# Optimization experiments

Hardware: AMD Instinct MI355X
Metric: run time of the kernel (lower is better)

## Reference

```python
import jax, jax.numpy as jnp
import numpy as np

B, D, S, SEQ_MAX = 8, 256, 1024, 1028  # seq_max = 4*seq_len+4 with seq_len=256
EPS = 1e-5


def setup_inputs() -> dict:
    key = jax.random.key(0)
    k1, k2 = jax.random.split(key, 2)
    x = jax.random.normal(k1, (B, D, S), dtype=jnp.float32)
    weight = jax.random.normal(k2, (D, SEQ_MAX, SEQ_MAX), dtype=jnp.float32)
    gamma = jnp.ones((D,), dtype=jnp.float32)   # LayerNorm weight
    beta = jnp.zeros((D,), dtype=jnp.float32)   # LayerNorm bias
    return {"x": x, "weight": weight, "gamma": gamma, "beta": beta}


def reference(x, weight, gamma, beta):
    s = x.shape[2]
    # strictly-causal per-channel mixing matrix (tril, diagonal=-1)
    w = jnp.tril(weight[:, :s, :s], k=-1)            # [d, s, s]
    # c[b,d,i] = sum_w x[b,d,w] * w[d,i,w]
    c = jax.nn.relu(jnp.einsum('bdw,diw->bdi', x, w))  # [b, d, s]
    # bracket(c, x, 0): elementwise multiplicative gating
    y = x + c * x
    # LayerNorm over the channel (d_model) axis, as in permute->LN->permute
    mu = jnp.mean(y, axis=1, keepdims=True)
    var = jnp.mean((y - mu) ** 2, axis=1, keepdims=True)
    yhat = (y - mu) * jax.lax.rsqrt(var + EPS)
    return yhat * gamma[None, :, None] + beta[None, :, None]
```

## Files before the change

kernel.cpp:

```cpp
#include <hip/hip_runtime.h>

#define SM 1028
#define D_ 256
#define S_ 1024
#define B_ 8

__global__ __launch_bounds__(256, 4)
void lie_mix_kernel(const float* __restrict__ x, const float* __restrict__ weight,
                    float* __restrict__ y) {
  int bid = blockIdx.x;
  int d = bid & 255;
  int bi = 15 - (bid >> 8);
  int i0 = bi << 6;

  __shared__ float xs[B_][S_];

  int t = threadIdx.x;
  int wlim4 = (i0 + 64) >> 2;
  for (int bb = 0; bb < B_; ++bb) {
    const float4* src = (const float4*)(x + ((size_t)bb * D_ + d) * S_);
    float4* dst = (float4*)(&xs[bb][0]);
    for (int idx = t; idx < wlim4; idx += 256) dst[idx] = src[idx];
  }
  __syncthreads();

  int lane = t & 63;
  int wid = t >> 6;
  int g = lane >> 4;
  int jj = lane & 15;
  int rbase = i0 + wid * 16 + g * 4;

  const float* wbase = weight + ((size_t)d * SM + rbase) * SM + 4 * jj;

  float acc[4][8];
#pragma unroll
  for (int k = 0; k < 4; ++k)
#pragma unroll
    for (int b = 0; b < 8; ++b) acc[k][b] = 0.f;

  int F = i0 >> 6;

  float4 wc[4];
#pragma unroll
  for (int k = 0; k < 4; ++k) wc[k] = *(const float4*)(wbase + (size_t)k * SM);

  for (int c = 0; c < F; ++c) {
    float4 wn[4];
    const float* p = wbase + (c + 1) * 64;
#pragma unroll
    for (int k = 0; k < 4; ++k) wn[k] = *(const float4*)(p + (size_t)k * SM);
    int w0 = c * 64;
#pragma unroll
    for (int b = 0; b < 8; ++b) {
      float4 xb = *(const float4*)&xs[b][w0 + 4 * jj];
#pragma unroll
      for (int k = 0; k < 4; ++k) {
        acc[k][b] += xb.x * wc[k].x;
        acc[k][b] += xb.y * wc[k].y;
        acc[k][b] += xb.z * wc[k].z;
        acc[k][b] += xb.w * wc[k].w;
      }
    }
#pragma unroll
    for (int k = 0; k < 4; ++k) wc[k] = wn[k];
  }

  {
    int lim_base = wid * 16 + g * 4;
    float4 wm[4];
#pragma unroll
    for (int k = 0; k < 4; ++k) {
      int lim = lim_base + k;
      wm[k].x = (4 * jj + 0 < lim) ? wc[k].x : 0.f;
      wm[k].y = (4 * jj + 1 < lim) ? wc[k].y : 0.f;
      wm[k].z = (4 * jj + 2 < lim) ? wc[k].z : 0.f;
      wm[k].w = (4 * jj + 3 < lim) ? wc[k].w : 0.f;
    }
#pragma unroll
    for (int b = 0; b < 8; ++b) {
      float4 xb = *(const float4*)&xs[b][i0 + 4 * jj];
#pragma unroll
      for (int k = 0; k < 4; ++k) {
        acc[k][b] += xb.x * wm[k].x;
        acc[k][b] += xb.y * wm[k].y;
        acc[k][b] += xb.z * wm[k].z;
        acc[k][b] += xb.w * wm[k].w;
      }
    }
  }

#pragma unroll
  for (int s = 1; s < 16; s <<= 1) {
#pragma unroll
    for (int k = 0; k < 4; ++k)
#pragma unroll
      for (int b = 0; b < 8; ++b)
        acc[k][b] += __shfl_xor(acc[k][b], s, 64);
  }

  if (jj < 8) {
#pragma unroll
    for (int k = 0; k < 4; ++k) {
      float v = acc[k][0];
#pragma unroll
      for (int b = 1; b < 8; ++b) v = (jj == b) ? acc[k][b] : v;
      float r = fmaxf(v, 0.f);
      float xv = xs[jj][rbase + k];
      y[((size_t)jj * D_ + d) * S_ + rbase + k] = xv * (1.f + r);
    }
  }
}

__global__ __launch_bounds__(256)
void ln_kernel(const float* __restrict__ y, const float* __restrict__ gamma,
               const float* __restrict__ beta, float* __restrict__ out) {
  __shared__ float tile[D_][33];
  __shared__ float ps[8][32];
  __shared__ float pq[8][32];
  __shared__ float mu[32];
  __shared__ float rs[32];
  int b = blockIdx.x >> 5;
  int s0 = (blockIdx.x & 31) << 5;
  int t = threadIdx.x;
  int sj = t & 31, dq = t >> 5;
  for (int dd = dq; dd < D_; dd += 8)
    tile[dd][sj] = y[((size_t)b * D_ + dd) * S_ + s0 + sj];
  __syncthreads();
  float sm = 0.f, sq = 0.f;
#pragma unroll 8
  for (int r = 0; r < 32; ++r) {
    float v = tile[dq * 32 + r][sj];
    sm += v;
    sq += v * v;
  }
  ps[dq][sj] = sm;
  pq[dq][sj] = sq;
  __syncthreads();
  if (t < 32) {
    float S = 0.f, Q = 0.f;
#pragma unroll
    for (int q = 0; q < 8; ++q) { S += ps[q][t]; Q += pq[q][t]; }
    float m = S * (1.f / 256.f);
    float var = Q * (1.f / 256.f) - m * m;
    mu[t] = m;
    rs[t] = rsqrtf(var + 1e-5f);
  }
  __syncthreads();
  for (int dd = dq; dd < D_; dd += 8) {
    float v = tile[dd][sj];
    out[((size_t)b * D_ + dd) * S_ + s0 + sj] =
        (v - mu[sj]) * rs[sj] * gamma[dd] + beta[dd];
  }
}

extern "C" void kernel_launch(void* const* d_in, const int* in_sizes, int n_in,
                              void* d_out, int out_size, void* d_ws, size_t ws_size,
                              hipStream_t stream) {
  const float* x = (const float*)d_in[0];
  const float* weight = (const float*)d_in[1];
  const float* gamma = (const float*)d_in[2];
  const float* beta = (const float*)d_in[3];
  float* out = (float*)d_out;
  float* y = (float*)d_ws;

  lie_mix_kernel<<<4096, 256, 0, stream>>>(x, weight, y);
  ln_kernel<<<256, 256, 0, stream>>>(y, gamma, beta, out);
}
```

Before: 129.1 us.

## Remap mix kernel so each wavefront reads full 1KB weight row segments

Changes the thread mapping of the causal mixing kernel so that all 64 lanes of a wavefront cover 256 contiguous weight columns of one row group, instead of 16 lanes covering 64 columns for four row groups. Each wave now loops over four row quads sequentially and reduces over the full wavefront with six shuffle stages. The x tile load is rounded up to a 256 multiple to match. The aim is wider, more coalesced weight reads. The cost is more shuffle reductions per output, extra lanes doing masked work in the diagonal block, and less parallel independent rows per wave.

Measured after the change: 216.7 us. 1.68x slower.

```diff
diff --git a/kernel.cpp b/kernel.cpp
--- a/kernel.cpp
+++ b/kernel.cpp
@@ -16,7 +16,7 @@
   __shared__ float xs[B_][S_];
 
   int t = threadIdx.x;
-  int wlim4 = (i0 + 64) >> 2;
+  int wlim4 = ((i0 + 64 + 255) & ~255) >> 2;
   for (int bb = 0; bb < B_; ++bb) {
     const float4* src = (const float4*)(x + ((size_t)bb * D_ + d) * S_);
     float4* dst = (float4*)(&xs[bb][0]);
@@ -26,87 +26,98 @@
 
   int lane = t & 63;
   int wid = t >> 6;
-  int g = lane >> 4;
-  int jj = lane & 15;
-  int rbase = i0 + wid * 16 + g * 4;
+  int e0 = lane << 2;
+  const size_t drow = (size_t)d * SM;
 
-  const float* wbase = weight + ((size_t)d * SM + rbase) * SM + 4 * jj;
+  for (int q = 0; q < 4; ++q) {
+    int rq = i0 + ((q << 2) + wid) << 2;
+    rq = i0 + (((q << 2) + wid) << 2);
+    const float* base = weight + (drow + rq) * (size_t)SM;
 
-  float acc[4][8];
+    float acc[4][8];
 #pragma unroll
-  for (int k = 0; k < 4; ++k)
+    for (int k = 0; k < 4; ++k)
 #pragma unroll
-    for (int b = 0; b < 8; ++b) acc[k][b] = 0.f;
+      for (int b = 0; b < 8; ++b) acc[k][b] = 0.f;
 
-  int F = i0 >> 6;
+    int cq = rq >> 8;
 
-  float4 wc[4];
+    float4 wc[4];
+    if (cq > 0) {
 #pragma unroll
-  for (int k = 0; k < 4; ++k) wc[k] = *(const float4*)(wbase + (size_t)k * SM);
+      for (int k = 0; k < 4; ++k)
+        wc[k] = *(const float4*)(base + (size_t)k * SM + e0);
+    }
+    for (int c = 0; c < cq; ++c) {
+      float4 wn[4];
+      if (c + 1 < cq) {
+        const float* p = base + ((c + 1) << 8) + e0;
+#pragma unroll
+        for (int k = 0; k < 4; ++k) wn[k] = *(const float4*)(p + (size_t)k * SM);
+      }
+      int w0 = c << 8;
+#pragma unroll
+      for (int b = 0; b < 8; ++b) {
+        float4 xb = *(const float4*)&xs[b][w0 + e0];
+#pragma unroll
+        for (int k = 0; k < 4; ++k) {
+          acc[k][b] += xb.x * wc[k].x;
+          acc[k][b] += xb.y * wc[k].y;
+          acc[k][b] += xb.z * wc[k].z;
+          acc[k][b] += xb.w * wc[k].w;
+        }
+      }
+      if (c + 1 < cq) {
+#pragma unroll
+        for (int k = 0; k < 4; ++k) wc[k] = wn[k];
+      }
+    }
 
-  for (int c = 0; c < F; ++c) {
-    float4 wn[4];
-    const float* p = wbase + (c + 1) * 64;
-#pragma unroll
-    for (int k = 0; k < 4; ++k) wn[k] = *(const float4*)(p + (size_t)k * SM);
-    int w0 = c * 64;
-#pragma unroll
-    for (int b = 0; b < 8; ++b) {
-      float4 xb = *(const float4*)&xs[b][w0 + 4 * jj];
+    {
+      int w0 = cq << 8;
+      float4 wm[4];
 #pragma unroll
       for (int k = 0; k < 4; ++k) {
-        acc[k][b] += xb.x * wc[k].x;
-        acc[k][b] += xb.y * wc[k].y;
-        acc[k][b] += xb.z * wc[k].z;
-        acc[k][b] += xb.w * wc[k].w;
+        int limit = rq + k - w0;
+        float4 v = make_float4(0.f, 0.f, 0.f, 0.f);
+        if (e0 < limit) v = *(const float4*)(base + (size_t)k * SM + w0 + e0);
+        if (e0 + 1 >= limit) v.y = 0.f;
+        if (e0 + 2 >= limit) v.z = 0.f;
+        if (e0 + 3 >= limit) v.w = 0.f;
+        wm[k] = v;
+      }
+#pragma unroll
+      for (int b = 0; b < 8; ++b) {
+        float4 xb = *(const float4*)&xs[b][w0 + e0];
+#pragma unroll
+        for (int k = 0; k < 4; ++k) {
+          acc[k][b] += xb.x * wm[k].x;
+          acc[k][b] += xb.y * wm[k].y;
+          acc[k][b] += xb.z * wm[k].z;
+          acc[k][b] += xb.w * wm[k].w;
+        }
       }
     }
-#pragma unroll
-    for (int k = 0; k < 4; ++k) wc[k] = wn[k];
-  }
-
-  {
-    int lim_base = wid * 16 + g * 4;
-    float4 wm[4];
-#pragma unroll
-    for (int k = 0; k < 4; ++k) {
-      int lim = lim_base + k;
-      wm[k].x = (4 * jj + 0 < lim) ? wc[k].x : 0.f;
-      wm[k].y = (4 * jj + 1 < lim) ? wc[k].y : 0.f;
-      wm[k].z = (4 * jj + 2 < lim) ? wc[k].z : 0.f;
-      wm[k].w = (4 * jj + 3 < lim) ? wc[k].w : 0.f;
-    }
-#pragma unroll
-    for (int b = 0; b < 8; ++b) {
-      float4 xb = *(const float4*)&xs[b][i0 + 4 * jj];
-#pragma unroll
-      for (int k = 0; k < 4; ++k) {
-        acc[k][b] += xb.x * wm[k].x;
-        acc[k][b] += xb.y * wm[k].y;
-        acc[k][b] += xb.z * wm[k].z;
-        acc[k][b] += xb.w * wm[k].w;
-      }
-    }
-  }
 
 #pragma unroll
-  for (int s = 1; s < 16; s <<= 1) {
+    for (int s = 1; s < 64; s <<= 1) {
+#pragma unroll
+      for (int k = 0; k < 4; ++k)
+#pragma unroll
+        for (int b = 0; b < 8; ++b)
+          acc[k][b] += __shfl_xor(acc[k][b], s, 64);
+    }
+
+    float v = 0.f;
 #pragma unroll
     for (int k = 0; k < 4; ++k)
 #pragma unroll
       for (int b = 0; b < 8; ++b)
-        acc[k][b] += __shfl_xor(acc[k][b], s, 64);
-  }
-
-  if (jj < 8) {
-#pragma unroll
-    for (int k = 0; k < 4; ++k) {
-      float v = acc[k][0];
-#pragma unroll
-      for (int b = 1; b < 8; ++b) v = (jj == b) ? acc[k][b] : v;
-      float r = fmaxf(v, 0.f);
-      float xv = xs[jj][rbase + k];
-      y[((size_t)jj * D_ + d) * S_ + rbase + k] = xv * (1.f + r);
+        v = (lane == (k << 3) + b) ? acc[k][b] : v;
+    if (lane < 32) {
+      int k = lane >> 3, b = lane & 7;
+      float xv = xs[b][rq + k];
+      y[((size_t)b * D_ + d) * S_ + rq + k] = xv * (1.f + fmaxf(v, 0.f));
     }
   }
 }
```

## Drop LDS staging of x, read x directly from global and vectorize output store

Applied to the files above, without the earlier changes.

Removes the 32KB shared-memory tile of x and its barrier, so each thread loads x float4s straight from global/L2 inside the loop. The explicit software prefetch of the next weight chunk is also removed, occupancy hint raised to 5 blocks, the diagonal weight load is masked, and the final output becomes a single float4 store. This aims to cut LDS use and raise occupancy, at the cost of redundant global reads of x across waves and losing the weight double-buffering.

Result: slower. 135.6 us (+5.0%).

```diff
diff --git a/kernel.cpp b/kernel.cpp
--- a/kernel.cpp
+++ b/kernel.cpp
@@ -5,7 +5,7 @@
 #define S_ 1024
 #define B_ 8
 
-__global__ __launch_bounds__(256, 4)
+__global__ __launch_bounds__(256, 5)
 void lie_mix_kernel(const float* __restrict__ x, const float* __restrict__ weight,
                     float* __restrict__ y) {
   int bid = blockIdx.x;
@@ -13,24 +13,16 @@
   int bi = 15 - (bid >> 8);
   int i0 = bi << 6;
 
-  __shared__ float xs[B_][S_];
-
   int t = threadIdx.x;
-  int wlim4 = (i0 + 64) >> 2;
-  for (int bb = 0; bb < B_; ++bb) {
-    const float4* src = (const float4*)(x + ((size_t)bb * D_ + d) * S_);
-    float4* dst = (float4*)(&xs[bb][0]);
-    for (int idx = t; idx < wlim4; idx += 256) dst[idx] = src[idx];
-  }
-  __syncthreads();
-
   int lane = t & 63;
   int wid = t >> 6;
   int g = lane >> 4;
   int jj = lane & 15;
-  int rbase = i0 + wid * 16 + g * 4;
+  int j4 = jj << 2;
+  int rbase = i0 + (wid << 4) + (g << 2);
 
-  const float* wbase = weight + ((size_t)d * SM + rbase) * SM + 4 * jj;
+  const float* wbase = weight + ((size_t)d * SM + rbase) * SM + j4;
+  const float* xd = x + ((size_t)d << 10);
 
   float acc[4][8];
 #pragma unroll
@@ -40,74 +32,88 @@
 
   int F = i0 >> 6;
 
-  float4 wc[4];
+  for (int c = 0; c < F; ++c) {
+    int w0 = c << 6;
+    float4 wc[4];
 #pragma unroll
-  for (int k = 0; k < 4; ++k) wc[k] = *(const float4*)(wbase + (size_t)k * SM);
-
-  for (int c = 0; c < F; ++c) {
-    float4 wn[4];
-    const float* p = wbase + (c + 1) * 64;
+    for (int k = 0; k < 4; ++k)
+      wc[k] = *(const float4*)(wbase + (size_t)k * SM + w0);
 #pragma unroll
-    for (int k = 0; k < 4; ++k) wn[k] = *(const float4*)(p + (size_t)k * SM);
-    int w0 = c * 64;
+    for (int h = 0; h < 2; ++h) {
+      float4 xb[4];
 #pragma unroll
-    for (int b = 0; b < 8; ++b) {
-      float4 xb = *(const float4*)&xs[b][w0 + 4 * jj];
+      for (int b = 0; b < 4; ++b)
+        xb[b] = *(const float4*)(xd + ((size_t)((h * 4 + b) << 8) << 10) + w0 + j4);
 #pragma unroll
-      for (int k = 0; k < 4; ++k) {
-        acc[k][b] += xb.x * wc[k].x;
-        acc[k][b] += xb.y * wc[k].y;
-        acc[k][b] += xb.z * wc[k].z;
-        acc[k][b] += xb.w * wc[k].w;
+      for (int b = 0; b < 4; ++b) {
+        int bb = h * 4 + b;
+#pragma unroll
+        for (int k = 0; k < 4; ++k) {
+          acc[k][bb] += xb[b].x * wc[k].x + xb[b].y * wc[k].y +
+                        xb[b].z * wc[k].z + xb[b].w * wc[k].w;
+        }
       }
     }
-#pragma unroll
-    for (int k = 0; k < 4; ++k) wc[k] = wn[k];
   }
 
   {
-    int lim_base = wid * 16 + g * 4;
+    int w0 = i0;
+    int lim0 = (wid << 4) + (g << 2);
     float4 wm[4];
 #pragma unroll
     for (int k = 0; k < 4; ++k) {
-      int lim = lim_base + k;
-      wm[k].x = (4 * jj + 0 < lim) ? wc[k].x : 0.f;
-      wm[k].y = (4 * jj + 1 < lim) ? wc[k].y : 0.f;
-      wm[k].z = (4 * jj + 2 < lim) ? wc[k].z : 0.f;
-      wm[k].w = (4 * jj + 3 < lim) ? wc[k].w : 0.f;
+      int lim = lim0 + k;
+      float4 v = make_float4(0.f, 0.f, 0.f, 0.f);
+      if (j4 < lim) v = *(const float4*)(wbase + (size_t)k * SM + w0);
+      if (j4 + 1 >= lim) v.y = 0.f;
+      if (j4 + 2 >= lim) v.z = 0.f;
+      if (j4 + 3 >= lim) v.w = 0.f;
+      wm[k] = v;
     }
 #pragma unroll
-    for (int b = 0; b < 8; ++b) {
-      float4 xb = *(const float4*)&xs[b][i0 + 4 * jj];
+    for (int h = 0; h < 2; ++h) {
+      float4 xb[4];
 #pragma unroll
-      for (int k = 0; k < 4; ++k) {
-        acc[k][b] += xb.x * wm[k].x;
-        acc[k][b] += xb.y * wm[k].y;
-        acc[k][b] += xb.z * wm[k].z;
-        acc[k][b] += xb.w * wm[k].w;
+      for (int b = 0; b < 4; ++b)
+        xb[b] = *(const float4*)(xd + ((size_t)((h * 4 + b) << 8) << 10) + w0 + j4);
+#pragma unroll
+      for (int b = 0; b < 4; ++b) {
+        int bb = h * 4 + b;
+#pragma unroll
+        for (int k = 0; k < 4; ++k) {
+          acc[k][bb] += xb[b].x * wm[k].x + xb[b].y * wm[k].y +
+                        xb[b].z * wm[k].z + xb[b].w * wm[k].w;
+        }
       }
     }
   }
 
 #pragma unroll
-  for (int s = 1; s < 16; s <<= 1) {
+  for (int s = 1; s < 16; s <<= 1)
 #pragma unroll
     for (int k = 0; k < 4; ++k)
 #pragma unroll
       for (int b = 0; b < 8; ++b)
         acc[k][b] += __shfl_xor(acc[k][b], s, 64);
-  }
 
   if (jj < 8) {
+    float4 o;
+    float v0 = 0.f, v1 = 0.f, v2 = 0.f, v3 = 0.f;
 #pragma unroll
-    for (int k = 0; k < 4; ++k) {
-      float v = acc[k][0];
-#pragma unroll
-      for (int b = 1; b < 8; ++b) v = (jj == b) ? acc[k][b] : v;
-      float r = fmaxf(v, 0.f);
-      float xv = xs[jj][rbase + k];
-      y[((size_t)jj * D_ + d) * S_ + rbase + k] = xv * (1.f + r);
+    for (int b = 0; b < 8; ++b) {
+      bool sel = (jj == b);
+      v0 = sel ? acc[0][b] : v0;
+      v1 = sel ? acc[1][b] : v1;
+      v2 = sel ? acc[2][b] : v2;
+      v3 = sel ? acc[3][b] : v3;
     }
+    const float* xp = xd + ((size_t)(jj << 8) << 10) + rbase;
+    float4 xv = *(const float4*)xp;
+    o.x = xv.x * (1.f + fmaxf(v0, 0.f));
+    o.y = xv.y * (1.f + fmaxf(v1, 0.f));
+    o.z = xv.z * (1.f + fmaxf(v2, 0.f));
+    o.w = xv.w * (1.f + fmaxf(v3, 0.f));
+    *(float4*)(y + ((size_t)(jj << 8) << 10) + ((size_t)d << 10) + rbase) = o;
   }
 }
 
@@ -139,10 +145,10 @@
   if (t < 32) {
     float S = 0.f, Q = 0.f;
 #pragma unroll
-    for (int q = 0; q < 8; ++q) { S += ps[q][t]; Q += pq[q][t]; }
-    float m = S * (1.f / 256.f);
-    float var = Q * (1.f / 256.f) - m * m;
-    mu[t] = m;
+    for (int qq = 0; qq < 8; ++qq) { S += ps[qq][t]; Q += pq[qq][t]; }
+    float mm = S * (1.f / 256.f);
+    float var = Q * (1.f / 256.f) - mm * mm;
+    mu[t] = mm;
     rs[t] = rsqrtf(var + 1e-5f);
   }
   __syncthreads();
```
